# Kernel tuning notes

Hardware: AMD Instinct MI355X
Metric: run time of the kernel (lower is better)

Reference implementation:

```python
import jax, jax.numpy as jnp
import numpy as np

B, T, D_MODEL, H = 2, 2048, 1024, 16
D_HEAD = D_MODEL // H


def setup_inputs() -> dict:
    key = jax.random.key(0)
    k1, k2, k3 = jax.random.split(key, 3)
    x = jax.random.normal(k1, (B, T, D_MODEL), dtype=jnp.float32)
    # Linear weights stored as (in, out); scale like torch default init roughly
    W_qkv = jax.random.normal(k2, (D_MODEL, 3 * D_MODEL), dtype=jnp.float32) / np.sqrt(D_MODEL)
    W_o = jax.random.normal(k3, (D_MODEL, D_MODEL), dtype=jnp.float32) / np.sqrt(D_MODEL)
    return {"x": x, "W_qkv": W_qkv, "W_o": W_o}


def reference(x, W_qkv, W_o):
    Bx, Tx, C = x.shape
    qkv = x @ W_qkv                                   # (B,T,3C)
    qkv = qkv.reshape(Bx, Tx, 3, H, D_HEAD)
    q = qkv[:, :, 0].transpose(0, 2, 1, 3)            # (B,H,T,D)
    k = qkv[:, :, 1].transpose(0, 2, 1, 3)
    v = qkv[:, :, 2].transpose(0, 2, 1, 3)
    scale = 1.0 / np.sqrt(D_HEAD).astype(np.float32)
    att = jnp.einsum('bhqd,bhkd->bhqk', q, k) * scale  # (B,H,T,T)
    causal = jnp.tril(jnp.ones((Tx, Tx), dtype=bool))
    att = jnp.where(causal[None, None], att, jnp.float32(-jnp.inf))
    w = jax.nn.softmax(att, axis=-1)
    out = jnp.einsum('bhqk,bhkd->bhqd', w, v)          # (B,H,T,D)
    out = out.transpose(0, 2, 1, 3).reshape(Bx, Tx, C)
    return out @ W_o
```

## Files before the change

### kernel.cpp

```cpp
#include <hip/hip_runtime.h>

typedef unsigned short u16;
typedef unsigned int u32;
typedef __bf16 bf16x8 __attribute__((ext_vector_type(8)));
typedef float f32x4 __attribute__((ext_vector_type(4)));

#define DEV __device__ __forceinline__

constexpr int BB = 2;
constexpr int TT = 2048;
constexpr int CD = 1024;
constexpr int HH = 16;
constexpr int DH = 64;
constexpr int BT = BB * TT;

#define QSCALE 0.18033688011112042f

DEV u16 f2bf(float f) {
    u32 u = __builtin_bit_cast(u32, f);
    u32 r = u + 0x7FFFu + ((u >> 16) & 1u);
    return (u16)(r >> 16);
}

DEV f32x4 mfma16(bf16x8 a, bf16x8 b, f32x4 c) {
    return __builtin_amdgcn_mfma_f32_16x16x32_bf16(a, b, c, 0, 0, 0);
}

DEV void gld_lds16(u16* lds, const u16* g) {
    __builtin_amdgcn_global_load_lds(
        (const __attribute__((address_space(1))) unsigned int*)g,
        (__attribute__((address_space(3))) unsigned int*)lds, 16, 0, 0);
}

__global__ __launch_bounds__(256)
void prep_kernel(const float* __restrict__ x, u16* __restrict__ xb,
                 const float* __restrict__ Wqkv, u16* __restrict__ WqkvT,
                 const float* __restrict__ Wo, u16* __restrict__ WoT) {
    const int tid = threadIdx.x;
    int blk = blockIdx.x;
    if (blk < 2048) {
        const int i = (blk * 256 + tid) * 8;
        float4 a = *(const float4*)&x[i];
        float4 b = *(const float4*)&x[i + 4];
        u16 t[8];
        t[0] = f2bf(a.x); t[1] = f2bf(a.y); t[2] = f2bf(a.z); t[3] = f2bf(a.w);
        t[4] = f2bf(b.x); t[5] = f2bf(b.y); t[6] = f2bf(b.z); t[7] = f2bf(b.w);
        *(uint4*)&xb[i] = *(const uint4*)t;
        return;
    }
    __shared__ u16 tile[32][33];
    const float* in; u16* out; int rows, cols, bx, by;
    if (blk < 5120) { blk -= 2048; in = Wqkv; out = WqkvT; rows = 1024; cols = 3072; bx = blk % 96; by = blk / 96; }
    else            { blk -= 5120; in = Wo;   out = WoT;   rows = 1024; cols = 1024; bx = blk % 32; by = blk / 32; }
    const int c0 = bx * 32, r0 = by * 32;
    const int tx = tid & 31, ty = tid >> 5;
    #pragma unroll
    for (int i = ty; i < 32; i += 8)
        tile[i][tx] = f2bf(in[(r0 + i) * cols + (c0 + tx)]);
    __syncthreads();
    #pragma unroll
    for (int i = ty; i < 32; i += 8)
        out[(c0 + i) * rows + (r0 + tx)] = tile[tx][i];
}

template <int EPI, int BN>
__global__ __launch_bounds__(256)
void gemm_bt(const u16* __restrict__ A, const u16* __restrict__ Bt,
             u16* __restrict__ out0, u16* __restrict__ out1,
             u16* __restrict__ out2, float* __restrict__ outf,
             int M, int N, int K) {
    constexpr int BM = 128, BK = 32, AST = 32;
    constexpr int NT = BN / 32;
    __shared__ alignas(16) u16 As[BM * AST];
    __shared__ alignas(16) u16 Bs[BN * AST];

    const int tid  = threadIdx.x;
    const int wave = tid >> 6, lane = tid & 63;
    const int quad = lane >> 4, l16 = lane & 15;
    const int wm = (wave & 1) * 64, wn = (wave >> 1) * (BN / 2);
    const int m0 = blockIdx.y * BM, n0 = blockIdx.x * BN;

    const int srowA = wave * 32 + (lane >> 2);
    const int srowB = wave * (BN / 4) + (lane >> 2);
    const int scol  = (lane & 3) * 8;
    const u16* ga0 = A  + (size_t)(m0 + srowA) * K + scol;
    const u16* ga1 = ga0 + (size_t)16 * K;
    const u16* gb0 = Bt + (size_t)(n0 + srowB) * K + scol;
    const u16* gb1 = gb0 + (size_t)16 * K;
    u16* la0 = As + wave * 1024;
    u16* la1 = As + wave * 1024 + 512;
    u16* lb0 = Bs + wave * (BN * 8);
    u16* lb1 = Bs + wave * (BN * 8) + 512;

    f32x4 acc[4][NT] = {};

    for (int k0 = 0; k0 < K; k0 += BK) {
        gld_lds16(la0, ga0 + k0);
        gld_lds16(la1, ga1 + k0);
        gld_lds16(lb0, gb0 + k0);
        if constexpr (BN == 128) gld_lds16(lb1, gb1 + k0);
        __syncthreads();

        bf16x8 fa[4], fb[NT];
        #pragma unroll
        for (int mt = 0; mt < 4; ++mt)
            fa[mt] = *(const bf16x8*)&As[(wm + mt * 16 + l16) * AST + quad * 8];
        #pragma unroll
        for (int nt = 0; nt < NT; ++nt)
            fb[nt] = *(const bf16x8*)&Bs[(wn + nt * 16 + l16) * AST + quad * 8];
        #pragma unroll
        for (int mt = 0; mt < 4; ++mt)
            #pragma unroll
            for (int nt = 0; nt < NT; ++nt)
                acc[mt][nt] = mfma16(fa[mt], fb[nt], acc[mt][nt]);
        __syncthreads();
    }

    #pragma unroll
    for (int mt = 0; mt < 4; ++mt) {
        #pragma unroll
        for (int nt = 0; nt < NT; ++nt) {
            #pragma unroll
            for (int reg = 0; reg < 4; ++reg) {
                const int r = m0 + wm + mt * 16 + quad * 4 + reg;
                const int c = n0 + wn + nt * 16 + l16;
                if (EPI == 0) {
                    outf[(size_t)r * N + c] = acc[mt][nt][reg];
                } else {
                    const int which = c >> 10;
                    const int cc = c & 1023;
                    const int h = cc >> 6, d = cc & 63;
                    const int b = r >> 11, t = r & 2047;
                    const int bh = b * HH + h;
                    if (which == 0) {
                        out0[((size_t)bh * TT + t) * DH + d] =
                            f2bf(acc[mt][nt][reg] * QSCALE);
                    } else if (which == 1) {
                        out1[((size_t)bh * TT + t) * DH + d] = f2bf(acc[mt][nt][reg]);
                    } else {
                        out2[((size_t)bh * DH + d) * TT + t] = f2bf(acc[mt][nt][reg]);
                    }
                }
            }
        }
    }
}

constexpr int KST = 72;

DEV void attn_step(const bf16x8 fk[4][2], const bf16x8 fv[2][4],
                   const bf16x8* fq, f32x4* Oacc,
                   float& m_i, float& l_i, bool diag,
                   int wave, int quad, int l16) {
    f32x4 st[4];
    #pragma unroll
    for (int nt = 0; nt < 4; ++nt) {
        f32x4 t = {};
        t = mfma16(fk[nt][0], fq[0], t);
        t = mfma16(fk[nt][1], fq[1], t);
        st[nt] = t;
    }

    if (diag) {
        const int qg = wave * 16 + l16;
        #pragma unroll
        for (int nt = 0; nt < 4; ++nt)
            #pragma unroll
            for (int reg = 0; reg < 4; ++reg) {
                const int kg = nt * 16 + quad * 4 + reg;
                st[nt][reg] = (kg <= qg) ? st[nt][reg] : -INFINITY;
            }
    }

    float vmax = st[0][0];
    #pragma unroll
    for (int nt = 0; nt < 4; ++nt)
        #pragma unroll
        for (int reg = 0; reg < 4; ++reg)
            vmax = fmaxf(vmax, st[nt][reg]);
    vmax = fmaxf(vmax, __shfl_xor(vmax, 16, 64));
    vmax = fmaxf(vmax, __shfl_xor(vmax, 32, 64));

    const float mnew = fmaxf(m_i, vmax);
    const float alpha = __builtin_amdgcn_exp2f(m_i - mnew);
    m_i = mnew;

    float vsum = 0.f;
    #pragma unroll
    for (int nt = 0; nt < 4; ++nt)
        #pragma unroll
        for (int reg = 0; reg < 4; ++reg) {
            const float p = __builtin_amdgcn_exp2f(st[nt][reg] - mnew);
            st[nt][reg] = p;
            vsum += p;
        }
    vsum += __shfl_xor(vsum, 16, 64);
    vsum += __shfl_xor(vsum, 32, 64);
    l_i = l_i * alpha + vsum;

    #pragma unroll
    for (int dt = 0; dt < 4; ++dt)
        #pragma unroll
        for (int reg = 0; reg < 4; ++reg)
            Oacc[dt][reg] *= alpha;

    #pragma unroll
    for (int pair = 0; pair < 2; ++pair) {
        u16 pa[8];
        #pragma unroll
        for (int j = 0; j < 4; ++j) {
            pa[j]     = f2bf(st[2 * pair][j]);
            pa[4 + j] = f2bf(st[2 * pair + 1][j]);
        }
        const bf16x8 pb = *(const bf16x8*)pa;
        #pragma unroll
        for (int dt = 0; dt < 4; ++dt)
            Oacc[dt] = mfma16(fv[pair][dt], pb, Oacc[dt]);
    }
}

__global__ __launch_bounds__(256, 2)
void attn_kernel(const u16* __restrict__ Q, const u16* __restrict__ Kb,
                 const u16* __restrict__ Vt, u16* __restrict__ O) {
    __shared__ alignas(16) u16 Ks[2][64 * KST];
    __shared__ alignas(16) u16 Vs[2][64 * KST];

    const int p = blockIdx.x;
    const int bh = blockIdx.y;
    const int qtA = 31 - p;
    const int qtB = p;
    const int jmax = qtA;

    const int tid = threadIdx.x;
    const int wave = tid >> 6, lane = tid & 63;
    const int quad = lane >> 4, l16 = lane & 15;

    const u16* Qh = Q  + (size_t)bh * TT * DH;
    const u16* Kh = Kb + (size_t)bh * TT * DH;
    const u16* Vh = Vt + (size_t)bh * DH * TT;

    const int rowA = qtA * 64 + wave * 16;
    const int rowB = qtB * 64 + wave * 16;

    bf16x8 fqA[2], fqB[2];
    fqA[0] = *(const bf16x8*)&Qh[(rowA + l16) * DH + quad * 8];
    fqA[1] = *(const bf16x8*)&Qh[(rowA + l16) * DH + 32 + quad * 8];
    fqB[0] = *(const bf16x8*)&Qh[(rowB + l16) * DH + quad * 8];
    fqB[1] = *(const bf16x8*)&Qh[(rowB + l16) * DH + 32 + quad * 8];

    f32x4 OA[4] = {}, OB[4] = {};
    float mA = -INFINITY, lA = 0.f, mB = -INFINITY, lB = 0.f;

    const int trow = tid >> 3;
    const int ic   = tid & 7;
    const int tcol = ic * 8;
    const int vc1 = 32 * (ic >> 2) + 16 * (ic & 1) + 4 * ((ic & 3) >> 1);
    uint4 kr0, kr1, vr0, vr1;

    auto load_chunk = [&](int j) {
        const u16* ks = Kh + (size_t)j * 64 * DH;
        kr0 = *(const uint4*)&ks[trow * DH + tcol];
        kr1 = *(const uint4*)&ks[(trow + 32) * DH + tcol];
        const u16* vs = Vh + (size_t)j * 64;
        vr0 = *(const uint4*)&vs[(size_t)trow * TT + tcol];
        vr1 = *(const uint4*)&vs[(size_t)(trow + 32) * TT + tcol];
    };
    auto write_chunk = [&](int buf) {
        *(uint4*)&Ks[buf][trow * KST + tcol]        = kr0;
        *(uint4*)&Ks[buf][(trow + 32) * KST + tcol] = kr1;
        *(uint2*)&Vs[buf][trow * KST + vc1]            = *(const uint2*)&vr0;
        *(uint2*)&Vs[buf][trow * KST + vc1 + 8]        = *((const uint2*)&vr0 + 1);
        *(uint2*)&Vs[buf][(trow + 32) * KST + vc1]     = *(const uint2*)&vr1;
        *(uint2*)&Vs[buf][(trow + 32) * KST + vc1 + 8] = *((const uint2*)&vr1 + 1);
    };

    load_chunk(0);
    write_chunk(0);

    for (int j = 0; j <= jmax; ++j) {
        const int cur = j & 1;
        __syncthreads();
        if (j < jmax) load_chunk(j + 1);

        bf16x8 fk[4][2], fv[2][4];
        #pragma unroll
        for (int nt = 0; nt < 4; ++nt) {
            fk[nt][0] = *(const bf16x8*)&Ks[cur][(nt * 16 + l16) * KST + quad * 8];
            fk[nt][1] = *(const bf16x8*)&Ks[cur][(nt * 16 + l16) * KST + 32 + quad * 8];
        }
        #pragma unroll
        for (int pair = 0; pair < 2; ++pair)
            #pragma unroll
            for (int dt = 0; dt < 4; ++dt)
                fv[pair][dt] = *(const bf16x8*)
                    &Vs[cur][(dt * 16 + l16) * KST + pair * 32 + quad * 8];

        attn_step(fk, fv, fqA, OA, mA, lA, (j == qtA), wave, quad, l16);
        if (j <= qtB)
            attn_step(fk, fv, fqB, OB, mB, lB, (j == qtB), wave, quad, l16);
        if (j < jmax) write_chunk(cur ^ 1);
    }

    const int b = bh >> 4, h = bh & 15;
    const float rA = 1.f / lA, rB = 1.f / lB;
    #pragma unroll
    for (int dt = 0; dt < 4; ++dt) {
        u16 oa[4], ob[4];
        #pragma unroll
        for (int reg = 0; reg < 4; ++reg) {
            oa[reg] = f2bf(OA[dt][reg] * rA);
            ob[reg] = f2bf(OB[dt][reg] * rB);
        }
        *(uint2*)&O[((size_t)(b * TT + rowA + l16)) * CD + h * DH + dt * 16 + quad * 4] =
            *(const uint2*)oa;
        *(uint2*)&O[((size_t)(b * TT + rowB + l16)) * CD + h * DH + dt * 16 + quad * 4] =
            *(const uint2*)ob;
    }
}

extern "C" void kernel_launch(void* const* d_in, const int* in_sizes, int n_in,
                              void* d_out, int out_size, void* d_ws, size_t ws_size,
                              hipStream_t stream) {
    (void)in_sizes; (void)n_in; (void)out_size; (void)ws_size;
    const float* x    = (const float*)d_in[0];
    const float* Wqkv = (const float*)d_in[1];
    const float* Wo   = (const float*)d_in[2];
    float* out = (float*)d_out;

    char* ws = (char*)d_ws;
    u16* xb    = (u16*)(ws + 0);
    u16* WqkvT = (u16*)(ws + (8u  << 20));
    u16* WoT   = (u16*)(ws + (14u << 20));
    u16* Qb    = (u16*)(ws + (16u << 20));
    u16* Kb    = (u16*)(ws + (24u << 20));
    u16* Vt    = (u16*)(ws + (32u << 20));
    u16* attn  = (u16*)(ws + (40u << 20));

    prep_kernel<<<6144, 256, 0, stream>>>(x, xb, Wqkv, WqkvT, Wo, WoT);

    gemm_bt<1, 128><<<dim3(3072 / 128, BT / 128), 256, 0, stream>>>(
        xb, WqkvT, Qb, Kb, Vt, nullptr, BT, 3072, CD);

    attn_kernel<<<dim3(16, BB * HH), 256, 0, stream>>>(Qb, Kb, Vt, attn);

    gemm_bt<0, 64><<<dim3(CD / 64, BT / 128), 256, 0, stream>>>(
        attn, WoT, nullptr, nullptr, nullptr, out, BT, CD, CD);
}
```

Measured before the change: 191.9 us.

## Add 256x256 double-buffered QKV GEMM kernel with direct-to-LDS loads

```diff
diff --git a/kernel.cpp b/kernel.cpp
--- a/kernel.cpp
+++ b/kernel.cpp
@@ -61,6 +61,156 @@
     #pragma unroll
     for (int i = ty; i < 32; i += 8)
         out[(c0 + i) * rows + (r0 + tx)] = tile[tx][i];
+}
+
+__global__ __launch_bounds__(512, 2)
+void gemm_qkv(const u16* __restrict__ A, const u16* __restrict__ Bt,
+              u16* __restrict__ Qo, u16* __restrict__ Ko, u16* __restrict__ Vo) {
+    __shared__ alignas(16) u16 As[2][256 * 64];
+    __shared__ alignas(16) u16 Bs[2][256 * 64];
+
+    const int tid = threadIdx.x;
+    const int wave = tid >> 6, lane = tid & 63;
+    const int quad = lane >> 4, l16 = lane & 15;
+    const int wm = (wave & 1) * 128, wn = (wave >> 1) * 64;
+
+    int bid = (int)blockIdx.x;
+    bid = (bid & 7) * 24 + (bid >> 3);
+    const int bx = bid % 12, by = bid / 12;
+    const int m0 = by * 256, n0 = bx * 256;
+
+    const int srow = wave * 8 + (lane >> 3);
+    const int schunk = ((lane & 7) ^ ((lane >> 3) & 7)) * 8;
+    const u16* gA = A  + (size_t)(m0 + srow) * CD + schunk;
+    const u16* gB = Bt + (size_t)(n0 + srow) * CD + schunk;
+
+    auto stage = [&](u16* ldsbuf, const u16* g, int h, int t) {
+        const u16* gg = g + (size_t)(h * 128) * CD + t * 64;
+        u16* ll = ldsbuf + (h * 128 + wave * 8) * 64;
+        gld_lds16(ll, gg);
+        gld_lds16(ll + 64 * 64, gg + (size_t)64 * CD);
+    };
+    auto rdA = [&](bf16x8* f, const u16* buf, int mh) {
+        #pragma unroll
+        for (int mt = 0; mt < 4; ++mt)
+            #pragma unroll
+            for (int ks = 0; ks < 2; ++ks) {
+                const int r = wm + mh * 64 + mt * 16 + l16;
+                f[mt * 2 + ks] = *(const bf16x8*)
+                    &buf[r * 64 + (((ks * 4 + quad) ^ (l16 & 7)) << 3)];
+            }
+    };
+    auto rdB = [&](bf16x8* f, const u16* buf, int nh) {
+        #pragma unroll
+        for (int nt = 0; nt < 2; ++nt)
+            #pragma unroll
+            for (int ks = 0; ks < 2; ++ks) {
+                const int r = wn + nh * 32 + nt * 16 + l16;
+                f[nt * 2 + ks] = *(const bf16x8*)
+                    &buf[r * 64 + (((ks * 4 + quad) ^ (l16 & 7)) << 3)];
+            }
+    };
+
+    f32x4 acc[8][4] = {};
+    auto mmq = [&](const bf16x8* fa, const bf16x8* fb, int mh, int nh) {
+        __builtin_amdgcn_s_setprio(1);
+        #pragma unroll
+        for (int ks = 0; ks < 2; ++ks)
+            #pragma unroll
+            for (int mt = 0; mt < 4; ++mt)
+                #pragma unroll
+                for (int nt = 0; nt < 2; ++nt)
+                    acc[mh * 4 + mt][nh * 2 + nt] =
+                        mfma16(fa[mt * 2 + ks], fb[nt * 2 + ks],
+                               acc[mh * 4 + mt][nh * 2 + nt]);
+        __builtin_amdgcn_s_setprio(0);
+    };
+
+    stage(As[0], gA, 0, 0); stage(As[0], gA, 1, 0);
+    stage(Bs[0], gB, 0, 0); stage(Bs[0], gB, 1, 0);
+    stage(As[1], gA, 0, 1); stage(As[1], gA, 1, 1);
+    stage(Bs[1], gB, 0, 1); stage(Bs[1], gB, 1, 1);
+    asm volatile("s_waitcnt vmcnt(8)" ::: "memory");
+    __builtin_amdgcn_s_barrier();
+
+    bf16x8 fa[8], fbL[4], fbH[4];
+
+    for (int i = 0; i < 8; ++i) {
+        rdA(fa, As[0], 0);
+        rdB(fbL, Bs[0], 0);
+        if (i >= 1) stage(As[1], gA, 0, 2 * i + 1);
+        __builtin_amdgcn_s_barrier();
+        asm volatile("s_waitcnt lgkmcnt(0)" ::: "memory");
+        mmq(fa, fbL, 0, 0);
+        __builtin_amdgcn_s_barrier();
+        rdB(fbH, Bs[0], 1);
+        if (i >= 1) stage(As[1], gA, 1, 2 * i + 1);
+        __builtin_amdgcn_s_barrier();
+        asm volatile("s_waitcnt lgkmcnt(0)" ::: "memory");
+        mmq(fa, fbH, 0, 1);
+        __builtin_amdgcn_s_barrier();
+        rdA(fa, As[0], 1);
+        if (i <= 6) stage(Bs[0], gB, 0, 2 * i + 2);
+        __builtin_amdgcn_s_barrier();
+        asm volatile("s_waitcnt lgkmcnt(0)" ::: "memory");
+        mmq(fa, fbH, 1, 1);
+        __builtin_amdgcn_s_barrier();
+        if (i <= 6) stage(Bs[0], gB, 1, 2 * i + 2);
+        __builtin_amdgcn_s_barrier();
+        mmq(fa, fbL, 1, 0);
+        if (i < 7) { asm volatile("s_waitcnt vmcnt(4)" ::: "memory"); }
+        else       { asm volatile("s_waitcnt vmcnt(0)" ::: "memory"); }
+        __builtin_amdgcn_s_barrier();
+        rdA(fa, As[1], 0);
+        rdB(fbL, Bs[1], 0);
+        if (i <= 6) stage(As[0], gA, 0, 2 * i + 2);
+        __builtin_amdgcn_s_barrier();
+        asm volatile("s_waitcnt lgkmcnt(0)" ::: "memory");
+        mmq(fa, fbL, 0, 0);
+        __builtin_amdgcn_s_barrier();
+        rdB(fbH, Bs[1], 1);
+        if (i <= 6) stage(As[0], gA, 1, 2 * i + 2);
+        __builtin_amdgcn_s_barrier();
+        asm volatile("s_waitcnt lgkmcnt(0)" ::: "memory");
+        mmq(fa, fbH, 0, 1);
+        __builtin_amdgcn_s_barrier();
+        rdA(fa, As[1], 1);
+        if (i <= 6) stage(Bs[1], gB, 0, 2 * i + 3);
+        __builtin_amdgcn_s_barrier();
+        asm volatile("s_waitcnt lgkmcnt(0)" ::: "memory");
+        mmq(fa, fbH, 1, 1);
+        __builtin_amdgcn_s_barrier();
+        if (i <= 6) stage(Bs[1], gB, 1, 2 * i + 3);
+        __builtin_amdgcn_s_barrier();
+        mmq(fa, fbL, 1, 0);
+        if (i < 7) { asm volatile("s_waitcnt vmcnt(4)" ::: "memory"); }
+        __builtin_amdgcn_s_barrier();
+    }
+
+    #pragma unroll
+    for (int mt = 0; mt < 8; ++mt) {
+        #pragma unroll
+        for (int nt = 0; nt < 4; ++nt) {
+            #pragma unroll
+            for (int reg = 0; reg < 4; ++reg) {
+                const int r = m0 + wm + mt * 16 + quad * 4 + reg;
+                const int c = n0 + wn + nt * 16 + l16;
+                const int which = c >> 10;
+                const int cc = c & 1023;
+                const int h = cc >> 6, d = cc & 63;
+                const int b = r >> 11, t = r & 2047;
+                const int bh = b * HH + h;
+                if (which == 0) {
+                    Qo[((size_t)bh * TT + t) * DH + d] =
+                        f2bf(acc[mt][nt][reg] * QSCALE);
+                } else if (which == 1) {
+                    Ko[((size_t)bh * TT + t) * DH + d] = f2bf(acc[mt][nt][reg]);
+                } else {
+                    Vo[((size_t)bh * DH + d) * TT + t] = f2bf(acc[mt][nt][reg]);
+                }
+            }
+        }
+    }
 }
 
 template <int EPI, int BN>
@@ -338,8 +488,7 @@
 
     prep_kernel<<<6144, 256, 0, stream>>>(x, xb, Wqkv, WqkvT, Wo, WoT);
 
-    gemm_bt<1, 128><<<dim3(3072 / 128, BT / 128), 256, 0, stream>>>(
-        xb, WqkvT, Qb, Kb, Vt, nullptr, BT, 3072, CD);
+    gemm_qkv<<<192, 512, 0, stream>>>(xb, WqkvT, Qb, Kb, Vt);
 
     attn_kernel<<<dim3(16, BB * HH), 256, 0, stream>>>(Qb, Kb, Vt, attn);
 
```

Result: slower. 206.6 us (+7.6%).

## Double-buffer GEMM LDS tiles and remap blocks for XCD locality

Applied to the files above, without the earlier changes.

```diff
diff --git a/kernel.cpp b/kernel.cpp
--- a/kernel.cpp
+++ b/kernel.cpp
@@ -63,22 +63,28 @@
         out[(c0 + i) * rows + (r0 + tx)] = tile[tx][i];
 }
 
-template <int EPI, int BN>
+template <int EPI, int BN, int GX>
 __global__ __launch_bounds__(256)
-void gemm_bt(const u16* __restrict__ A, const u16* __restrict__ Bt,
+void gemm_db(const u16* __restrict__ A, const u16* __restrict__ Bt,
              u16* __restrict__ out0, u16* __restrict__ out1,
              u16* __restrict__ out2, float* __restrict__ outf,
              int M, int N, int K) {
     constexpr int BM = 128, BK = 32, AST = 32;
     constexpr int NT = BN / 32;
-    __shared__ alignas(16) u16 As[BM * AST];
-    __shared__ alignas(16) u16 Bs[BN * AST];
+    constexpr int NBLK = GX * 32;
+    constexpr int CPX = NBLK / 8;
+    __shared__ alignas(16) u16 As[2][BM * AST];
+    __shared__ alignas(16) u16 Bs[2][BN * AST];
 
     const int tid  = threadIdx.x;
     const int wave = tid >> 6, lane = tid & 63;
     const int quad = lane >> 4, l16 = lane & 15;
     const int wm = (wave & 1) * 64, wn = (wave >> 1) * (BN / 2);
-    const int m0 = blockIdx.y * BM, n0 = blockIdx.x * BN;
+
+    int bid = (int)blockIdx.x;
+    bid = (bid & 7) * CPX + (bid >> 3);
+    const int bx = bid % GX, by = bid / GX;
+    const int m0 = by * BM, n0 = bx * BN;
 
     const int srowA = wave * 32 + (lane >> 2);
     const int srowB = wave * (BN / 4) + (lane >> 2);
@@ -87,27 +93,31 @@
     const u16* ga1 = ga0 + (size_t)16 * K;
     const u16* gb0 = Bt + (size_t)(n0 + srowB) * K + scol;
     const u16* gb1 = gb0 + (size_t)16 * K;
-    u16* la0 = As + wave * 1024;
-    u16* la1 = As + wave * 1024 + 512;
-    u16* lb0 = Bs + wave * (BN * 8);
-    u16* lb1 = Bs + wave * (BN * 8) + 512;
+
+    auto stage = [&](int buf, int k0) {
+        gld_lds16(&As[buf][wave * 1024],           ga0 + k0);
+        gld_lds16(&As[buf][wave * 1024 + 512],     ga1 + k0);
+        gld_lds16(&Bs[buf][wave * (BN * 8)],       gb0 + k0);
+        if constexpr (BN == 128)
+            gld_lds16(&Bs[buf][wave * (BN * 8) + 512], gb1 + k0);
+    };
 
     f32x4 acc[4][NT] = {};
 
-    for (int k0 = 0; k0 < K; k0 += BK) {
-        gld_lds16(la0, ga0 + k0);
-        gld_lds16(la1, ga1 + k0);
-        gld_lds16(lb0, gb0 + k0);
-        if constexpr (BN == 128) gld_lds16(lb1, gb1 + k0);
-        __syncthreads();
+    stage(0, 0);
+    __syncthreads();
+
+    int cur = 0;
+    for (int k0 = 0; k0 < K; k0 += BK, cur ^= 1) {
+        if (k0 + BK < K) stage(cur ^ 1, k0 + BK);
 
         bf16x8 fa[4], fb[NT];
         #pragma unroll
         for (int mt = 0; mt < 4; ++mt)
-            fa[mt] = *(const bf16x8*)&As[(wm + mt * 16 + l16) * AST + quad * 8];
+            fa[mt] = *(const bf16x8*)&As[cur][(wm + mt * 16 + l16) * AST + quad * 8];
         #pragma unroll
         for (int nt = 0; nt < NT; ++nt)
-            fb[nt] = *(const bf16x8*)&Bs[(wn + nt * 16 + l16) * AST + quad * 8];
+            fb[nt] = *(const bf16x8*)&Bs[cur][(wn + nt * 16 + l16) * AST + quad * 8];
         #pragma unroll
         for (int mt = 0; mt < 4; ++mt)
             #pragma unroll
@@ -338,11 +348,11 @@
 
     prep_kernel<<<6144, 256, 0, stream>>>(x, xb, Wqkv, WqkvT, Wo, WoT);
 
-    gemm_bt<1, 128><<<dim3(3072 / 128, BT / 128), 256, 0, stream>>>(
+    gemm_db<1, 128, 24><<<768, 256, 0, stream>>>(
         xb, WqkvT, Qb, Kb, Vt, nullptr, BT, 3072, CD);
 
     attn_kernel<<<dim3(16, BB * HH), 256, 0, stream>>>(Qb, Kb, Vt, attn);
 
-    gemm_bt<0, 64><<<dim3(CD / 64, BT / 128), 256, 0, stream>>>(
+    gemm_db<0, 64, 16><<<512, 256, 0, stream>>>(
         attn, WoT, nullptr, nullptr, nullptr, out, BT, CD, CD);
 }
```

Measured after the change: 185.9 us. 1.03x faster.
